# Kernel tuning notes

Measured on AMD Instinct MI355X. Metric: run time of the kernel, lower is better.

The kernel has to match this reference:

```python
import jax, jax.numpy as jnp
import numpy as np

B, S, D = 8, 2048, 1024          # batch, seq, d_model
E, H = 32, 128                   # n_experts_ffn, d_expert_ffn
SHARED, K = 2, 4                 # n_expert_shared_ffn, k_ffn (routed top-k)
R = E - SHARED                   # n_expert_routed_ffn


def setup_inputs() -> dict:
    key = jax.random.key(0)
    ks = jax.random.split(key, 5)
    token_stream = jax.random.normal(ks[0], (B, S, D), jnp.float32)
    selection_input = jax.random.normal(ks[1], (B, S, D), jnp.float32)
    # init scaling mirrors reset_parameters (std_scale = 1)
    keys = jax.random.normal(ks[2], (E, D, H), jnp.float32) / np.sqrt(D)
    values = jax.random.normal(ks[3], (E, H, D), jnp.float32) / np.sqrt(E * H)
    expert_sel = jax.random.normal(ks[4], (E, D), jnp.float32) / np.sqrt(D)
    bias_ffn = jnp.zeros((E,), jnp.float32)
    return {
        "token_stream": token_stream,
        "selection_input": selection_input,
        "keys": keys,
        "values": values,
        "expert_sel": expert_sel,
        "bias_ffn": bias_ffn,
    }


def reference(token_stream, selection_input, keys, values, expert_sel, bias_ffn):
    # Router: sigmoid affinity over all experts. [B,S,E]
    affinity = jax.nn.sigmoid(jnp.einsum("bsd,ed->bse", selection_input, expert_sel))

    # Top-k over routed experts only (bias-corrected scores pick INDICES only).
    routed_scores = affinity[..., :R] + bias_ffn[:R]
    _, sel_routed = jax.lax.top_k(routed_scores, K)            # [B,S,K] int32
    shared = jnp.broadcast_to(jnp.arange(R, E, dtype=sel_routed.dtype),
                              sel_routed.shape[:-1] + (SHARED,))
    sel = jnp.concatenate([sel_routed, shared], axis=-1)        # [B,S,K+SHARED]

    # Gather the (unbiased) affinities of the selected experts.
    aff_sel = jnp.take_along_axis(affinity, sel, axis=-1)       # [B,S,K+SHARED]

    # Per-token dense combine weight over experts: w[b,s,e] = affinity if e selected else 0.
    # (selected indices are distinct: topk indices in [0,R), shared in [R,E))
    w = jnp.sum(jax.nn.one_hot(sel, E, dtype=affinity.dtype) * aff_sel[..., None],
                axis=-2)                                        # [B,S,E]

    # Expert FFN: cvmm(x, sel, keys) -> silu -> cvmm(., sel, values) weighted by affinity.
    # Dense-masked equivalent: compute all experts, zero out unselected via w.
    h = jax.nn.silu(jnp.einsum("bsd,edh->bseh", token_stream, keys))  # [B,S,E,H]
    out = jnp.einsum("bseh,bse,ehd->bsd", h, w, values)               # [B,S,D]
    return out, sel
```

## Files before the change

kernel.cpp:

```cpp
#include <hip/hip_runtime.h>
#include <math.h>

#define NTOK   16384
#define DDIM   1024
#define HDIM   128
#define NEXP   32
#define NROUTE 30
#define TOPK   4
#define TS     64
#define NJOBS_F 1696
#define CPX_F   212
#define SLAB   ((size_t)NTOK * DDIM)
#define NB_FUSED 5120

typedef short bf16x8 __attribute__((ext_vector_type(8)));
typedef float f32x16 __attribute__((ext_vector_type(16)));
typedef unsigned int u32x4 __attribute__((ext_vector_type(4)));
typedef unsigned short u16;

__device__ __forceinline__ float sigmoidf_(float x) { return 1.f / (1.f + expf(-x)); }

__device__ __forceinline__ u16 f2bf(float x) {
  unsigned u = __float_as_uint(x);
  u += 0x7fffu + ((u >> 16) & 1u);
  return (u16)(u >> 16);
}
__device__ __forceinline__ float bf2f(u16 v) {
  return __uint_as_float(((unsigned)v) << 16);
}

__device__ __forceinline__ f32x16 mfma32(uint4 a, uint4 b, f32x16 c) {
  union { uint4 u; bf16x8 h; } A, B;
  A.u = a; B.u = b;
  return __builtin_amdgcn_mfma_f32_32x32x16_bf16(A.h, B.h, c, 0, 0, 0);
}

__device__ __forceinline__ void gload16(const void* g, void* l) {
  __builtin_amdgcn_global_load_lds(
      (const __attribute__((address_space(1))) unsigned int*)g,
      (__attribute__((address_space(3))) unsigned int*)l, 16, 0, 0);
}

__device__ __forceinline__ void lgkm_bar() {
  asm volatile("s_waitcnt lgkmcnt(0)\ns_barrier" ::: "memory");
}

__global__ __launch_bounds__(256, 2) void prep_router_kernel(
    const float* __restrict__ X, u16* __restrict__ Xb,
    const float* __restrict__ K, u16* __restrict__ Kf,
    const float* __restrict__ V, u16* __restrict__ Vf,
    const float* __restrict__ SI, const float* __restrict__ ES,
    const float* __restrict__ bias, float* __restrict__ out_sel,
    float* __restrict__ w6, int* __restrict__ sel_e, int* __restrict__ counts)
{
  __shared__ __align__(16) char lds[66048];
  const int tid = threadIdx.x;

  if ((blockIdx.x % 10) == 9) {
    const int rb = blockIdx.x / 10;
    const int wave = tid >> 6, lane = tid & 63;
    const int tok0 = rb * 32 + wave * 8;
    float (*pbuf)[65] = ((float (*)[65])lds) + wave * 32;
    float (*aff)[33]  = (float (*)[33])(lds + 33280);

    float x[8][16];
#pragma unroll
    for (int t = 0; t < 8; ++t) {
      const float* xp = SI + (size_t)(tok0 + t) * DDIM + lane * 16;
#pragma unroll
      for (int q = 0; q < 4; ++q) {
        const float4 v = *(const float4*)(xp + q * 4);
        x[t][q*4+0]=v.x; x[t][q*4+1]=v.y; x[t][q*4+2]=v.z; x[t][q*4+3]=v.w;
      }
    }

#pragma unroll
    for (int g = 0; g < 8; ++g) {
#pragma unroll
      for (int ei = 0; ei < 4; ++ei) {
        const int e = g * 4 + ei;
        float es[16];
        const float* ep = ES + (size_t)e * DDIM + lane * 16;
#pragma unroll
        for (int q = 0; q < 4; ++q) {
          const float4 v = *(const float4*)(ep + q * 4);
          es[q*4+0]=v.x; es[q*4+1]=v.y; es[q*4+2]=v.z; es[q*4+3]=v.w;
        }
#pragma unroll
        for (int t = 0; t < 8; ++t) {
          float p = 0.f;
#pragma unroll
          for (int u = 0; u < 16; ++u) p = fmaf(x[t][u], es[u], p);
          pbuf[ei * 8 + t][lane] = p;
        }
      }
      const int pr = lane & 31, hf = lane >> 5;
      const float* src = &pbuf[pr][hf * 32];
      float4 s4 = make_float4(0.f, 0.f, 0.f, 0.f);
#pragma unroll
      for (int j = 0; j < 8; ++j) {
        const float4 v = *(const float4*)(src + j * 4);
        s4.x += v.x; s4.y += v.y; s4.z += v.z; s4.w += v.w;
      }
      float s = (s4.x + s4.y) + (s4.z + s4.w);
      s += __shfl_xor(s, 32, 64);
      if (hf == 0) aff[wave * 8 + (pr & 7)][g * 4 + (pr >> 3)] = s;
    }

    if (lane < 8) {
      const int tok = tok0 + lane;
      float af[NEXP];
#pragma unroll
      for (int e2 = 0; e2 < NEXP; ++e2)
        af[e2] = sigmoidf_(aff[wave * 8 + lane][e2]);
      float sc[NROUTE];
#pragma unroll
      for (int e2 = 0; e2 < NROUTE; ++e2) sc[e2] = af[e2] + bias[e2];
      unsigned used = 0u;
      int idx[6];
#pragma unroll
      for (int j = 0; j < TOPK; ++j) {
        float bv = -1e30f; int best = 0;
#pragma unroll
        for (int e2 = 0; e2 < NROUTE; ++e2)
          if (!((used >> e2) & 1u) && sc[e2] > bv) { bv = sc[e2]; best = e2; }
        used |= (1u << best);
        idx[j] = best;
      }
      idx[4] = 30; idx[5] = 31;
#pragma unroll
      for (int j = 0; j < 6; ++j) {
        out_sel[(size_t)tok * 6 + j] = (float)idx[j];
        w6[(size_t)tok * 6 + j] = af[idx[j]];
      }
#pragma unroll
      for (int j = 0; j < TOPK; ++j) {
        sel_e[(size_t)tok * TOPK + j] = idx[j];
        atomicAdd(&counts[j * NEXP + idx[j]], 1);
      }
    }
    return;
  }

  int b = blockIdx.x - (blockIdx.x + 1) / 10;
  float (*t)[129] = (float (*)[129])lds;

  if (b < 4096) {
    const size_t base = ((size_t)b * 256 + tid) * 16;
    u16 v[16];
#pragma unroll
    for (int i = 0; i < 4; ++i) {
      const float4 f = *(const float4*)(X + base + i * 4);
      v[i*4+0] = f2bf(f.x); v[i*4+1] = f2bf(f.y);
      v[i*4+2] = f2bf(f.z); v[i*4+3] = f2bf(f.w);
    }
    *(uint4*)(Xb + base) = *(const uint4*)v;
    *(uint4*)(Xb + base + 8) = *(const uint4*)(v + 8);
    return;
  }
  b -= 4096;
  if (b < 256) {
    const int kc = b & 7, e = b >> 3;
#pragma unroll
    for (int i = 0; i < 64; ++i) {
      const int g = tid + i * 256;
      const int d = g >> 7, h = g & 127;
      t[d][h] = K[((size_t)e * DDIM + kc * 128 + d) * HDIM + h];
    }
    __syncthreads();
    u16* dst = Kf + ((size_t)e * 8 + kc) * 16384;
#pragma unroll
    for (int i = 0; i < 64; ++i) {
      const int f = tid + i * 256;
      const int s = f >> 11, wn = (f >> 9) & 3, l = (f >> 3) & 63, j = f & 7;
      const int khalf = l >> 5, l31 = l & 31;
      dst[f] = f2bf(t[(s * 2 + khalf) * 8 + j][wn * 32 + l31]);
    }
    return;
  }
  b -= 256;
  {
    const int dc = b & 7, e = b >> 3;
#pragma unroll
    for (int i = 0; i < 64; ++i) {
      const int g = tid + i * 256;
      const int h = g >> 7, dl = g & 127;
      t[h][dl] = V[((size_t)e * HDIM + h) * DDIM + dc * 128 + dl];
    }
    __syncthreads();
    u16* dst = Vf + ((size_t)e * 8 + dc) * 16384;
#pragma unroll
    for (int i = 0; i < 64; ++i) {
      const int f = tid + i * 256;
      const int s = f >> 11, wn = (f >> 9) & 3, l = (f >> 3) & 63, j = f & 7;
      const int khalf = l >> 5, l31 = l & 31;
      dst[f] = f2bf(t[(s * 2 + khalf) * 8 + j][wn * 32 + l31]);
    }
  }
}

__global__ __launch_bounds__(256) void scan_kernel(const int* __restrict__ counts,
                                                   int* __restrict__ offsets,
                                                   int4* __restrict__ jm)
{
  __shared__ int c4[30][4];
  __shared__ int off4[30][4];
  __shared__ int nch[32];
  __shared__ int joff[31];
  const int tid = threadIdx.x;

  if (tid < 4) {
    int off = 0;
    for (int e = 0; e < NROUTE; ++e) {
      const int c = counts[tid * NEXP + e];
      offsets[tid * NEXP + e] = off;
      c4[e][tid] = c; off4[e][tid] = off;
      off += c;
    }
  }
  __syncthreads();
  if (tid < NROUTE) {
    int n = 0;
#pragma unroll
    for (int r = 0; r < 4; ++r) n += (c4[tid][r] + TS - 1) / TS;
    nch[tid] = n;
  }
  __syncthreads();
  if (tid == 0) {
    int run = 0;
    for (int e = 0; e < NROUTE; ++e) { joff[e] = run; run += nch[e]; }
    joff[NROUTE] = run;
  }
  __syncthreads();
  const int rt = joff[NROUTE];

  if (tid < NROUTE) {
    const int e = tid;
    int idx = joff[e];
    for (int r = 0; r < 4; ++r) {
      const int c = c4[e][r];
      for (int ch = 0; ch * TS < c; ++ch)
        jm[idx++] = make_int4(e, off4[e][r] + ch * TS, min(TS, c - ch * TS), r);
    }
  }
  for (int i = tid; i < 512; i += 256)
    jm[rt + i] = make_int4(30 + (i >> 8), (i & 255) * TS, TS, 4 + (i >> 8));
  for (int i = rt + 512 + tid; i < NJOBS_F; i += 256)
    jm[i] = make_int4(0, 0, 0, 0);
}

__global__ __launch_bounds__(256) void scatter_kernel(
    const int* __restrict__ sel_e, const float* __restrict__ w6,
    const int* __restrict__ offsets, int* __restrict__ cursor,
    int* __restrict__ list_tok, float* __restrict__ list_w)
{
  const int t = blockIdx.x * 256 + threadIdx.x;
  if (t >= NTOK) return;
#pragma unroll
  for (int j = 0; j < TOPK; ++j) {
    const int e   = sel_e[(size_t)t * TOPK + j];
    const int pos = atomicAdd(&cursor[j * NEXP + e], 1);
    const int dst = j * NTOK + offsets[j * NEXP + e] + pos;
    list_tok[dst] = t;
    list_w[dst]   = w6[(size_t)t * 6 + j];
  }
  list_tok[4 * NTOK + t] = t; list_w[4 * NTOK + t] = w6[(size_t)t * 6 + 4];
  list_tok[5 * NTOK + t] = t; list_w[5 * NTOK + t] = w6[(size_t)t * 6 + 5];
}

__device__ __forceinline__ void loadb(uint4* b, const u16* __restrict__ base,
                                      int c, int wid, int lane) {
#pragma unroll
  for (int s = 0; s < 8; ++s)
    b[s] = *(const uint4*)(base + (size_t)(((c * 8 + s) * 4 + wid) * 512) + lane * 8);
}

__global__ __launch_bounds__(256, 2) void ffn_kernel(
    const u16* __restrict__ Xb, const u16* __restrict__ Kf, const u16* __restrict__ Vf,
    const int4* __restrict__ jm, const int* __restrict__ list_tok,
    const float* __restrict__ list_w, u16* __restrict__ part)
{
  __shared__ __align__(16) u16 Xs[2][8192];
  __shared__ __align__(16) u16 Hs[TS * 128];
  __shared__ int   s_tok[TS];
  __shared__ float s_w[TS];

  const int bid = blockIdx.x;
  const int4 J = jm[(bid & 7) * CPX_F + (bid >> 3)];
  const int nrow = J.z;
  if (nrow == 0) return;
  const int e = J.x, base = J.y, rank = J.w;
  const int tid = threadIdx.x;
  const int wid = tid >> 6, lane = tid & 63;
  const int l31 = lane & 31, khalf = lane >> 5;
  const int sx = l31 & 15;

  const u16* Kf_e = Kf + (size_t)e * 131072;
  const u16* Vf_e = Vf + (size_t)e * 131072;
  const int*   lt  = list_tok + rank * NTOK + base;
  const float* lww = list_w  + rank * NTOK + base;

  size_t srcoff[4];
#pragma unroll
  for (int u = 0; u < 4; ++u) {
    const int r  = wid * 16 + u * 4 + (lane >> 4);
    const int rr = (r < nrow) ? r : 0;
    srcoff[u] = (size_t)lt[rr] * DDIM + (size_t)(((lane & 15) ^ (r & 15)) << 3);
  }

  #define STAGE_A(kc_, buf_) do { \
    _Pragma("unroll") \
    for (int u_ = 0; u_ < 4; ++u_) \
      gload16(Xb + srcoff[u_] + (kc_) * 128, &Xs[buf_][(wid * 16 + u_ * 4) * 128]); \
  } while (0)

  uint4 bb[2][8];
  STAGE_A(0, 0);
  loadb(bb[0], Kf_e, 0, wid, lane);

  if (tid < TS) {
    int t = 0; float w = 0.f;
    if (tid < nrow) { t = lt[tid]; w = lww[tid]; }
    s_tok[tid] = t; s_w[tid] = w;
  }
  lgkm_bar();

  f32x16 acc0, acc1;
#pragma unroll
  for (int i = 0; i < 16; ++i) { acc0[i] = 0.f; acc1[i] = 0.f; }

#pragma unroll
  for (int kc = 0; kc < 8; ++kc) {
    const int cur = kc & 1;
    asm volatile("s_barrier" ::: "memory");
    __builtin_amdgcn_sched_barrier(0);
    if (kc < 7) { STAGE_A(kc + 1, cur ^ 1); loadb(bb[cur ^ 1], Kf_e, kc + 1, wid, lane); }
    else        { loadb(bb[cur ^ 1], Vf_e, 0, wid, lane); }
    if (kc < 7) asm volatile("s_waitcnt vmcnt(12)" ::: "memory");
    else        asm volatile("s_waitcnt vmcnt(8)"  ::: "memory");
    asm volatile("s_barrier" ::: "memory");
    __builtin_amdgcn_sched_barrier(0);
#pragma unroll
    for (int s = 0; s < 8; ++s) {
      const int so = (((s * 2 + khalf) ^ sx) << 3);
      const uint4 a0 = *(const uint4*)(&Xs[cur][l31 * 128 + so]);
      const uint4 a1 = *(const uint4*)(&Xs[cur][(32 + l31) * 128 + so]);
      acc0 = mfma32(a0, bb[cur][s], acc0);
      acc1 = mfma32(a1, bb[cur][s], acc1);
    }
  }

  {
    const int hcol = wid * 32 + l31;
#pragma unroll
    for (int r = 0; r < 16; ++r) {
      const int row0 = (r & 3) + 8 * (r >> 2) + 4 * khalf;
      float v0 = acc0[r];
      v0 = v0 / (1.f + expf(-v0)) * s_w[row0];
      Hs[row0 * 128 + ((((hcol >> 3) ^ (row0 & 15)) << 3) | (hcol & 7))] = f2bf(v0);
      const int row1 = row0 + 32;
      float v1 = acc1[r];
      v1 = v1 / (1.f + expf(-v1)) * s_w[row1];
      Hs[row1 * 128 + ((((hcol >> 3) ^ (row1 & 15)) << 3) | (hcol & 7))] = f2bf(v1);
    }
  }
  lgkm_bar();

  uint4 a20[8], a21[8];
#pragma unroll
  for (int s = 0; s < 8; ++s) {
    a20[s] = *(const uint4*)(Hs + l31 * 128 + (((s * 2 + khalf) ^ sx) << 3));
    a21[s] = *(const uint4*)(Hs + (32 + l31) * 128 + (((s * 2 + khalf) ^ sx) << 3));
  }

  unsigned ob0[16], ob1[16]; bool ov0[16], ov1[16];
#pragma unroll
  for (int r = 0; r < 16; ++r) {
    const int row0 = (r & 3) + 8 * (r >> 2) + 4 * khalf;
    const int row1 = row0 + 32;
    ov0[r] = row0 < nrow; ov1[r] = row1 < nrow;
    ob0[r] = (unsigned)s_tok[row0] * DDIM;
    ob1[r] = (unsigned)s_tok[row1] * DDIM;
  }

  u16* pp = part + (size_t)rank * SLAB;

#pragma unroll
  for (int dc = 0; dc < 8; ++dc) {
    const int cur = dc & 1;
    if (dc < 7) loadb(bb[cur ^ 1], Vf_e, dc + 1, wid, lane);
    f32x16 o0, o1;
#pragma unroll
    for (int i = 0; i < 16; ++i) { o0[i] = 0.f; o1[i] = 0.f; }
#pragma unroll
    for (int s = 0; s < 8; ++s) {
      o0 = mfma32(a20[s], bb[cur][s], o0);
      o1 = mfma32(a21[s], bb[cur][s], o1);
    }
    const int col = dc * 128 + wid * 32 + l31;
#pragma unroll
    for (int r = 0; r < 16; ++r) {
      if (ov0[r]) __builtin_nontemporal_store(f2bf(o0[r]), &pp[(size_t)ob0[r] + col]);
      if (ov1[r]) __builtin_nontemporal_store(f2bf(o1[r]), &pp[(size_t)ob1[r] + col]);
    }
  }
  #undef STAGE_A
}

__global__ __launch_bounds__(256) void reduce_kernel(const u16* __restrict__ part,
                                                     float* __restrict__ out)
{
  const size_t i8 = ((size_t)blockIdx.x * 256 + threadIdx.x) * 8;
  float s[8];
#pragma unroll
  for (int j = 0; j < 8; ++j) s[j] = 0.f;
#pragma unroll
  for (int r = 0; r < 6; ++r) {
    const u32x4 v = __builtin_nontemporal_load((const u32x4*)(part + r * SLAB + i8));
#pragma unroll
    for (int q = 0; q < 4; ++q) {
      s[q*2+0] += __uint_as_float((v[q] & 0xffffu) << 16);
      s[q*2+1] += __uint_as_float(v[q] & 0xffff0000u);
    }
  }
  float4 o0 = make_float4(s[0], s[1], s[2], s[3]);
  float4 o1 = make_float4(s[4], s[5], s[6], s[7]);
  *(float4*)(out + i8) = o0;
  *(float4*)(out + i8 + 4) = o1;
}

extern "C" void kernel_launch(void* const* d_in, const int* in_sizes, int n_in,
                              void* d_out, int out_size, void* d_ws, size_t ws_size,
                              hipStream_t stream)
{
  const float* X    = (const float*)d_in[0];
  const float* SI   = (const float*)d_in[1];
  const float* keys = (const float*)d_in[2];
  const float* vals = (const float*)d_in[3];
  const float* ES   = (const float*)d_in[4];
  const float* bias = (const float*)d_in[5];
  float* out = (float*)d_out;
  float* out_sel = out + SLAB;

  char* ws = (char*)d_ws;
  int*   counts   = (int*)(ws + 0);
  int*   cursor   = (int*)(ws + 512);
  int*   offsets  = (int*)(ws + 1024);
  int4*  jm       = (int4*)(ws + 2048);
  int*   list_tok = (int*)(ws + 57344);
  float* list_w   = (float*)(ws + 450560);
  float* w6       = (float*)(ws + 919552);
  int*   sel_e    = (int*)(ws + 1312768);
  u16*   Xb       = (u16*)(ws + 1576960);
  u16*   Kf       = (u16*)(ws + 35131392);
  u16*   Vf       = (u16*)(ws + 43520000);
  u16*   part     = (u16*)(ws + 51908608);

  hipMemsetAsync(counts, 0, 1024, stream);

  prep_router_kernel<<<NB_FUSED, 256, 0, stream>>>(X, Xb, keys, Kf, vals, Vf,
                                                   SI, ES, bias, out_sel, w6,
                                                   sel_e, counts);
  scan_kernel<<<1, 256, 0, stream>>>(counts, offsets, jm);
  scatter_kernel<<<NTOK / 256, 256, 0, stream>>>(sel_e, w6, offsets, cursor, list_tok, list_w);
  ffn_kernel<<<NJOBS_F, 256, 0, stream>>>(Xb, Kf, Vf, jm, list_tok, list_w, part);
  reduce_kernel<<<SLAB / (256 * 8), 256, 0, stream>>>(part, out);
}
```

Baseline: 398.8 us.

## Restructure router into 64-token blocks with double-buffered async LDS staging

```diff
diff --git a/kernel.cpp b/kernel.cpp
--- a/kernel.cpp
+++ b/kernel.cpp
@@ -11,7 +11,8 @@
 #define NJOBS_F 1696
 #define CPX_F   212
 #define SLAB   ((size_t)NTOK * DDIM)
-#define NB_FUSED 5120
+#define NB_ROUTER 256
+#define NB_FUSED  (NB_ROUTER + 4608)
 
 typedef short bf16x8 __attribute__((ext_vector_type(8)));
 typedef float f32x16 __attribute__((ext_vector_type(16)));
@@ -56,66 +57,74 @@
   __shared__ __align__(16) char lds[66048];
   const int tid = threadIdx.x;
 
-  if ((blockIdx.x % 10) == 9) {
-    const int rb = blockIdx.x / 10;
-    const int wave = tid >> 6, lane = tid & 63;
-    const int tok0 = rb * 32 + wave * 8;
-    float (*pbuf)[65] = ((float (*)[65])lds) + wave * 32;
-    float (*aff)[33]  = (float (*)[33])(lds + 33280);
-
-    float x[8][16];
-#pragma unroll
-    for (int t = 0; t < 8; ++t) {
-      const float* xp = SI + (size_t)(tok0 + t) * DDIM + lane * 16;
-#pragma unroll
-      for (int q = 0; q < 4; ++q) {
-        const float4 v = *(const float4*)(xp + q * 4);
-        x[t][q*4+0]=v.x; x[t][q*4+1]=v.y; x[t][q*4+2]=v.z; x[t][q*4+3]=v.w;
+  if (blockIdx.x < NB_ROUTER) {
+    const int wid = tid >> 6, lane = tid & 63;
+    const int tok0 = blockIdx.x * 64;
+    float* xs  = (float*)lds;
+    float* aff = (float*)(lds + 16384);
+
+    size_t rsrc[2];
+    int    ldst[2];
+#pragma unroll
+    for (int u = 0; u < 2; ++u) {
+      const int t = wid * 16 + u * 8 + (lane >> 3);
+      rsrc[u] = (size_t)(tok0 + t) * DDIM + (size_t)(((lane & 7) ^ (t & 7)) * 4);
+      ldst[u] = (wid * 16 + u * 8) * 32;
+    }
+    const int e0 = __builtin_amdgcn_readfirstlane(wid * 8);
+    const float* esp = ES + (size_t)e0 * DDIM;
+
+    #define STAGE_R(c_, buf_) do { \
+      _Pragma("unroll") \
+      for (int u_ = 0; u_ < 2; ++u_) \
+        gload16(SI + rsrc[u_] + (c_) * 32, xs + (buf_) * 2048 + ldst[u_]); \
+    } while (0)
+
+    float acc[8];
+#pragma unroll
+    for (int e = 0; e < 8; ++e) acc[e] = 0.f;
+
+    STAGE_R(0, 0);
+
+    for (int c = 0; c < 32; ++c) {
+      const int cur = c & 1;
+      asm volatile("s_barrier" ::: "memory");
+      __builtin_amdgcn_sched_barrier(0);
+      if (c < 31) {
+        STAGE_R(c + 1, cur ^ 1);
+        asm volatile("s_waitcnt vmcnt(2)" ::: "memory");
+      } else {
+        asm volatile("s_waitcnt vmcnt(0)" ::: "memory");
       }
-    }
-
-#pragma unroll
-    for (int g = 0; g < 8; ++g) {
-#pragma unroll
-      for (int ei = 0; ei < 4; ++ei) {
-        const int e = g * 4 + ei;
-        float es[16];
-        const float* ep = ES + (size_t)e * DDIM + lane * 16;
-#pragma unroll
-        for (int q = 0; q < 4; ++q) {
-          const float4 v = *(const float4*)(ep + q * 4);
-          es[q*4+0]=v.x; es[q*4+1]=v.y; es[q*4+2]=v.z; es[q*4+3]=v.w;
-        }
-#pragma unroll
-        for (int t = 0; t < 8; ++t) {
-          float p = 0.f;
-#pragma unroll
-          for (int u = 0; u < 16; ++u) p = fmaf(x[t][u], es[u], p);
-          pbuf[ei * 8 + t][lane] = p;
-        }
+      asm volatile("s_barrier" ::: "memory");
+      __builtin_amdgcn_sched_barrier(0);
+
+      float x[32];
+#pragma unroll
+      for (int j = 0; j < 8; ++j)
+        *(float4*)(x + j * 4) =
+            *(const float4*)(xs + cur * 2048 + lane * 32 + ((j ^ (lane & 7)) * 4));
+#pragma unroll
+      for (int kk = 0; kk < 32; ++kk) {
+        const float xv = x[kk];
+#pragma unroll
+        for (int e = 0; e < 8; ++e)
+          acc[e] = fmaf(xv, esp[(size_t)e * DDIM + c * 32 + kk], acc[e]);
       }
-      const int pr = lane & 31, hf = lane >> 5;
-      const float* src = &pbuf[pr][hf * 32];
-      float4 s4 = make_float4(0.f, 0.f, 0.f, 0.f);
-#pragma unroll
-      for (int j = 0; j < 8; ++j) {
-        const float4 v = *(const float4*)(src + j * 4);
-        s4.x += v.x; s4.y += v.y; s4.z += v.z; s4.w += v.w;
-      }
-      float s = (s4.x + s4.y) + (s4.z + s4.w);
-      s += __shfl_xor(s, 32, 64);
-      if (hf == 0) aff[wave * 8 + (pr & 7)][g * 4 + (pr >> 3)] = s;
-    }
-
-    if (lane < 8) {
+    }
+
+#pragma unroll
+    for (int e = 0; e < 8; ++e) aff[lane * 33 + e0 + e] = acc[e];
+    __syncthreads();
+
+    if (wid == 0) {
       const int tok = tok0 + lane;
-      float af[NEXP];
 #pragma unroll
       for (int e2 = 0; e2 < NEXP; ++e2)
-        af[e2] = sigmoidf_(aff[wave * 8 + lane][e2]);
+        aff[lane * 33 + e2] = sigmoidf_(aff[lane * 33 + e2]);
       float sc[NROUTE];
 #pragma unroll
-      for (int e2 = 0; e2 < NROUTE; ++e2) sc[e2] = af[e2] + bias[e2];
+      for (int e2 = 0; e2 < NROUTE; ++e2) sc[e2] = aff[lane * 33 + e2] + bias[e2];
       unsigned used = 0u;
       int idx[6];
 #pragma unroll
@@ -131,7 +140,7 @@
 #pragma unroll
       for (int j = 0; j < 6; ++j) {
         out_sel[(size_t)tok * 6 + j] = (float)idx[j];
-        w6[(size_t)tok * 6 + j] = af[idx[j]];
+        w6[(size_t)tok * 6 + j] = aff[lane * 33 + idx[j]];
       }
 #pragma unroll
       for (int j = 0; j < TOPK; ++j) {
@@ -139,10 +148,11 @@
         atomicAdd(&counts[j * NEXP + idx[j]], 1);
       }
     }
+    #undef STAGE_R
     return;
   }
 
-  int b = blockIdx.x - (blockIdx.x + 1) / 10;
+  int b = blockIdx.x - NB_ROUTER;
   float (*t)[129] = (float (*)[129])lds;
 
   if (b < 4096) {
```

Measured after the change: 486.5 us. 1.22x slower.

## Coalesce router loads, aggregate counts in LDS, place router blocks first

Applied to the files above, without the earlier changes.

```diff
diff --git a/kernel.cpp b/kernel.cpp
--- a/kernel.cpp
+++ b/kernel.cpp
@@ -11,7 +11,8 @@
 #define NJOBS_F 1696
 #define CPX_F   212
 #define SLAB   ((size_t)NTOK * DDIM)
-#define NB_FUSED 5120
+#define NB_ROUTER 512
+#define NB_FUSED  (NB_ROUTER + 4608)
 
 typedef short bf16x8 __attribute__((ext_vector_type(8)));
 typedef float f32x16 __attribute__((ext_vector_type(16)));
@@ -56,21 +57,23 @@
   __shared__ __align__(16) char lds[66048];
   const int tid = threadIdx.x;
 
-  if ((blockIdx.x % 10) == 9) {
-    const int rb = blockIdx.x / 10;
+  if (blockIdx.x < NB_ROUTER) {
     const int wave = tid >> 6, lane = tid & 63;
-    const int tok0 = rb * 32 + wave * 8;
+    const int tok0 = blockIdx.x * 32 + wave * 8;
     float (*pbuf)[65] = ((float (*)[65])lds) + wave * 32;
     float (*aff)[33]  = (float (*)[33])(lds + 33280);
+    int* hist = (int*)(lds + 37504);
+
+    if (tid < 128) hist[tid] = 0;
 
     float x[8][16];
 #pragma unroll
     for (int t = 0; t < 8; ++t) {
-      const float* xp = SI + (size_t)(tok0 + t) * DDIM + lane * 16;
-#pragma unroll
-      for (int q = 0; q < 4; ++q) {
-        const float4 v = *(const float4*)(xp + q * 4);
-        x[t][q*4+0]=v.x; x[t][q*4+1]=v.y; x[t][q*4+2]=v.z; x[t][q*4+3]=v.w;
+      const float* xp = SI + (size_t)(tok0 + t) * DDIM + lane * 4;
+#pragma unroll
+      for (int s = 0; s < 4; ++s) {
+        const float4 v = *(const float4*)(xp + s * 256);
+        x[t][s*4+0]=v.x; x[t][s*4+1]=v.y; x[t][s*4+2]=v.z; x[t][s*4+3]=v.w;
       }
     }
 
@@ -80,11 +83,11 @@
       for (int ei = 0; ei < 4; ++ei) {
         const int e = g * 4 + ei;
         float es[16];
-        const float* ep = ES + (size_t)e * DDIM + lane * 16;
-#pragma unroll
-        for (int q = 0; q < 4; ++q) {
-          const float4 v = *(const float4*)(ep + q * 4);
-          es[q*4+0]=v.x; es[q*4+1]=v.y; es[q*4+2]=v.z; es[q*4+3]=v.w;
+        const float* ep = ES + (size_t)e * DDIM + lane * 4;
+#pragma unroll
+        for (int s = 0; s < 4; ++s) {
+          const float4 v = *(const float4*)(ep + s * 256);
+          es[s*4+0]=v.x; es[s*4+1]=v.y; es[s*4+2]=v.z; es[s*4+3]=v.w;
         }
 #pragma unroll
         for (int t = 0; t < 8; ++t) {
@@ -106,6 +109,7 @@
       s += __shfl_xor(s, 32, 64);
       if (hf == 0) aff[wave * 8 + (pr & 7)][g * 4 + (pr >> 3)] = s;
     }
+    __syncthreads();
 
     if (lane < 8) {
       const int tok = tok0 + lane;
@@ -136,13 +140,18 @@
 #pragma unroll
       for (int j = 0; j < TOPK; ++j) {
         sel_e[(size_t)tok * TOPK + j] = idx[j];
-        atomicAdd(&counts[j * NEXP + idx[j]], 1);
-      }
+        atomicAdd(&hist[j * NEXP + idx[j]], 1);
+      }
+    }
+    __syncthreads();
+    if (tid < 128) {
+      const int c = hist[tid];
+      if (c) atomicAdd(&counts[tid], c);
     }
     return;
   }
 
-  int b = blockIdx.x - (blockIdx.x + 1) / 10;
+  int b = blockIdx.x - NB_ROUTER;
   float (*t)[129] = (float (*)[129])lds;
 
   if (b < 4096) {
```

New measurement: 336.6 us. 15.6% less time.
